# Performance work log

Measured on AMD Instinct MI355X. Metric: run time of the kernel, lower is better.

The kernel has to match this reference:

```python
import jax, jax.numpy as jnp
import numpy as np

B, C, H, W = 2, 256, 64, 64
D = 4  # max dilation ring


def _offsets():
    offs = [(0, 0)]
    for s in range(1, D + 1):
        for a in (-s, 0, s):
            for b in (-s, 0, s):
                if a != 0 or b != 0:
                    offs.append((a, b))
    return np.array(offs, dtype=np.int32)  # (33, 2)


def setup_inputs() -> dict:
    key = jax.random.key(0)
    k1, k2, k3, k4 = jax.random.split(key, 4)
    scale = 1.0 / np.sqrt(C)
    return {
        "Ft": jax.random.normal(k1, (B, C, H, W), dtype=jnp.float32),
        "Ft_epsilon": jax.random.normal(k2, (B, C, H, W), dtype=jnp.float32),
        "Wf": jax.random.normal(k3, (256, C), dtype=jnp.float32) * scale,
        "bf": jnp.zeros((256,), dtype=jnp.float32),
        "Wg": jax.random.normal(k4, (256, C), dtype=jnp.float32) * scale,
        "bg": jnp.zeros((256,), dtype=jnp.float32),
    }


def reference(Ft, Ft_epsilon, Wf, bf, Wg, bg):
    # 1x1 conv embeddings
    Ef = jnp.einsum("bchw,oc->bohw", Ft, Wf) + bf[None, :, None, None]          # f(Ft)
    Eg = jnp.einsum("bchw,oc->bohw", Ft_epsilon, Wg) + bg[None, :, None, None]  # g(Ft_eps)

    offs = _offsets()                                  # (K,2), K=33
    dx = jnp.asarray(offs[:, 0])[:, None, None]        # (K,1,1)
    dy = jnp.asarray(offs[:, 1])[:, None, None]
    xs = jnp.arange(H)[None, :, None] + dx             # (K,H,1)
    ys = jnp.arange(W)[None, None, :] + dy             # (K,1,W)
    valid = ((xs >= 0) & (xs < H)) & ((ys >= 0) & (ys < W))  # (K,H,W)
    xc = jnp.clip(xs, 0, H - 1)
    yc = jnp.clip(ys, 0, W - 1)

    # gather neighbor embeddings and features: (B,C,K,H,W)
    Ef_n = Ef[:, :, xc, yc]
    Ft_n = Ft[:, :, xc, yc]

    # affinity of center embedding with each neighbor embedding
    aff = jnp.einsum("bchw,bckhw->bkhw", Eg, Ef_n)     # (B,K,H,W)
    aff = jnp.where(valid[None], aff, -jnp.inf)        # clip out-of-bounds neighbors
    w = jax.nn.softmax(aff, axis=1)                    # (B,K,H,W); center always valid

    out = jnp.einsum("bkhw,bckhw->bchw", w, Ft_n)      # (B,C,H,W)
    return out
```

## Files before the change

kernel.cpp:

```cpp
#include <hip/hip_runtime.h>
#include <math.h>

typedef __attribute__((ext_vector_type(4))) float f4;

__device__ __forceinline__ int iclamp(int x, int lo, int hi) { return min(max(x, lo), hi); }

__device__ constexpr int DXC[33] = {0, -1,-1,-1,0,0,1,1,1, -2,-2,-2,0,0,2,2,2, -3,-3,-3,0,0,3,3,3, -4,-4,-4,0,0,4,4,4};
__device__ constexpr int DYC[33] = {0, -1,0,1,-1,1,-1,0,1, -2,0,2,-2,2,-2,0,2, -3,0,3,-3,3,-3,0,3, -4,0,4,-4,4,-4,0,4};

__global__ __launch_bounds__(256) void mat_M(
    const float* __restrict__ Wf, const float* __restrict__ Wg,
    const float* __restrict__ bg, float* __restrict__ Mt, float* __restrict__ r)
{
    __shared__ float Sf[32][33], Sg[32][33];
    __shared__ float Rs[32][9];
    const int c1b = blockIdx.x * 32, c2b = blockIdx.y * 32;
    const int tid = threadIdx.x;
    const int tx = tid & 15, ty = tid >> 4;
    float acc[2][2] = {};
    for (int ko = 0; ko < 256; ko += 32) {
        #pragma unroll
        for (int i = 0; i < 4; ++i) {
            int f = i * 256 + tid, o = f >> 5, c = f & 31;
            Sf[o][c] = Wf[(ko + o) * 256 + c1b + c];
            Sg[o][c] = Wg[(ko + o) * 256 + c2b + c];
        }
        __syncthreads();
        #pragma unroll
        for (int o = 0; o < 32; ++o) {
            float f0 = Sf[o][ty * 2], f1 = Sf[o][ty * 2 + 1];
            float g0 = Sg[o][tx * 2], g1 = Sg[o][tx * 2 + 1];
            acc[0][0] += f0 * g0; acc[0][1] += f0 * g1;
            acc[1][0] += f1 * g0; acc[1][1] += f1 * g1;
        }
        __syncthreads();
    }
    #pragma unroll
    for (int i = 0; i < 2; ++i)
        #pragma unroll
        for (int j = 0; j < 2; ++j)
            Mt[(size_t)(c2b + tx * 2 + j) * 256 + c1b + ty * 2 + i] = acc[i][j];

    if (blockIdx.y == 0) {
        const int c1l = tid & 31, og = tid >> 5;
        float s = 0.f;
        #pragma unroll 8
        for (int o = og * 32; o < og * 32 + 32; ++o)
            s += Wf[o * 256 + c1b + c1l] * bg[o];
        Rs[c1l][og] = s;
        __syncthreads();
        if (tid < 32) {
            float t = 0.f;
            #pragma unroll
            for (int j = 0; j < 8; ++j) t += Rs[tid][j];
            r[c1b + tid] = t;
        }
    }
}

__global__ __launch_bounds__(256, 2) void gemm_G(
    const float* __restrict__ Mt, const float* __restrict__ r,
    const float* __restrict__ FtE, float* __restrict__ G)
{
    __shared__ float Ms[256][64];
    const int bid = blockIdx.x;
    const int bn = bid & 63, bm = (bid >> 6) & 3, b = bid >> 8;
    const int tid = threadIdx.x;
    const int tn = tid & 15, tm = tid >> 4;
    const int m0 = bm * 64;
    const int m0g = m0 + tm * 4;
    const int n0g = bn * 64 + tn * 4;
    const float* X = FtE + (size_t)b * 1048576 + n0g;

    #pragma unroll
    for (int i = 0; i < 16; ++i) {
        int f = i * 256 + tid;
        int k = f >> 4, mi = f & 15;
        *(f4*)&Ms[k][mi * 4] = *(const f4*)&Mt[(size_t)k * 256 + m0 + mi * 4];
    }
    __syncthreads();

    f4 acc0 = {0.f,0.f,0.f,0.f}, acc1 = acc0, acc2 = acc0, acc3 = acc0;

    for (int kc = 0; kc < 256; kc += 8) {
        f4 x0 = *(const f4*)(X + (size_t)(kc + 0) * 4096);
        f4 x1 = *(const f4*)(X + (size_t)(kc + 1) * 4096);
        f4 x2 = *(const f4*)(X + (size_t)(kc + 2) * 4096);
        f4 x3 = *(const f4*)(X + (size_t)(kc + 3) * 4096);
        f4 x4 = *(const f4*)(X + (size_t)(kc + 4) * 4096);
        f4 x5 = *(const f4*)(X + (size_t)(kc + 5) * 4096);
        f4 x6 = *(const f4*)(X + (size_t)(kc + 6) * 4096);
        f4 x7 = *(const f4*)(X + (size_t)(kc + 7) * 4096);
        f4 a0 = *(const f4*)&Ms[kc + 0][tm * 4];
        f4 a1 = *(const f4*)&Ms[kc + 1][tm * 4];
        f4 a2 = *(const f4*)&Ms[kc + 2][tm * 4];
        f4 a3 = *(const f4*)&Ms[kc + 3][tm * 4];
        f4 a4 = *(const f4*)&Ms[kc + 4][tm * 4];
        f4 a5 = *(const f4*)&Ms[kc + 5][tm * 4];
        f4 a6 = *(const f4*)&Ms[kc + 6][tm * 4];
        f4 a7 = *(const f4*)&Ms[kc + 7][tm * 4];
        acc0 += x0 * a0.x; acc1 += x0 * a0.y; acc2 += x0 * a0.z; acc3 += x0 * a0.w;
        acc0 += x1 * a1.x; acc1 += x1 * a1.y; acc2 += x1 * a1.z; acc3 += x1 * a1.w;
        acc0 += x2 * a2.x; acc1 += x2 * a2.y; acc2 += x2 * a2.z; acc3 += x2 * a2.w;
        acc0 += x3 * a3.x; acc1 += x3 * a3.y; acc2 += x3 * a3.z; acc3 += x3 * a3.w;
        acc0 += x4 * a4.x; acc1 += x4 * a4.y; acc2 += x4 * a4.z; acc3 += x4 * a4.w;
        acc0 += x5 * a5.x; acc1 += x5 * a5.y; acc2 += x5 * a5.z; acc3 += x5 * a5.w;
        acc0 += x6 * a6.x; acc1 += x6 * a6.y; acc2 += x6 * a6.z; acc3 += x6 * a6.w;
        acc0 += x7 * a7.x; acc1 += x7 * a7.y; acc2 += x7 * a7.z; acc3 += x7 * a7.w;
    }

    float* Gp = G + (size_t)b * 1048576;
    {
        f4 v;
        v = acc0 + r[m0g + 0]; *(f4*)&Gp[(size_t)(m0g + 0) * 4096 + n0g] = v;
        v = acc1 + r[m0g + 1]; *(f4*)&Gp[(size_t)(m0g + 1) * 4096 + n0g] = v;
        v = acc2 + r[m0g + 2]; *(f4*)&Gp[(size_t)(m0g + 2) * 4096 + n0g] = v;
        v = acc3 + r[m0g + 3]; *(f4*)&Gp[(size_t)(m0g + 3) * 4096 + n0g] = v;
    }
}

template<bool LO, bool HI>
__device__ __forceinline__ void ldwin(float* wn, const float* Lb, int rd, int ch, int wq) {
    const float* p = &Lb[(rd * 8 + ch) * 72 + wq * 4];
    if constexpr (LO) { f4 v = *(const f4*)p;       wn[0]=v.x; wn[1]=v.y; wn[2]=v.z;  wn[3]=v.w; }
    {                   f4 v = *(const f4*)(p + 4); wn[4]=v.x; wn[5]=v.y; wn[6]=v.z;  wn[7]=v.w; }
    if constexpr (HI) { f4 v = *(const f4*)(p + 8); wn[8]=v.x; wn[9]=v.y; wn[10]=v.z; wn[11]=v.w; }
}

template<int DY>
__device__ __forceinline__ void fmadd4(f4& a, const f4& eg, const float* wn) {
    a.x += eg.x * wn[4 + DY];
    a.y += eg.y * wn[5 + DY];
    a.z += eg.z * wn[6 + DY];
    a.w += eg.w * wn[7 + DY];
}

template<int KQ>
__device__ __forceinline__ void aff_compute(const float* Lb, int wq, int cg, f4* acc)
{
    #pragma unroll
    for (int chi = 0; chi < 2; ++chi) {
        const int ch = cg * 2 + chi;
        f4 eg = *(const f4*)&Lb[(72 + ch) * 72 + 4 + wq * 4];
        float wn[12];
        if constexpr (KQ == 0) {
            ldwin<true,true>(wn, Lb, 0, ch, wq);
            fmadd4<-4>(acc[0], eg, wn); fmadd4<0>(acc[1], eg, wn); fmadd4<4>(acc[2], eg, wn);
            ldwin<true,true>(wn, Lb, 1, ch, wq);
            fmadd4<-3>(acc[3], eg, wn); fmadd4<0>(acc[4], eg, wn); fmadd4<3>(acc[5], eg, wn);
            ldwin<true,true>(wn, Lb, 2, ch, wq);
            fmadd4<-2>(acc[6], eg, wn); fmadd4<0>(acc[7], eg, wn); fmadd4<2>(acc[8], eg, wn);
        } else if constexpr (KQ == 1) {
            ldwin<true,true>(wn, Lb, 3, ch, wq);
            fmadd4<-1>(acc[0], eg, wn); fmadd4<0>(acc[1], eg, wn); fmadd4<1>(acc[2], eg, wn);
            ldwin<true,false>(wn, Lb, 4, ch, wq);
            fmadd4<-1>(acc[3], eg, wn); fmadd4<-2>(acc[4], eg, wn);
            fmadd4<-3>(acc[5], eg, wn); fmadd4<-4>(acc[6], eg, wn);
        } else if constexpr (KQ == 2) {
            ldwin<false,true>(wn, Lb, 4, ch, wq);
            fmadd4<0>(acc[0], eg, wn); fmadd4<1>(acc[1], eg, wn); fmadd4<2>(acc[2], eg, wn);
            fmadd4<3>(acc[3], eg, wn); fmadd4<4>(acc[4], eg, wn);
            ldwin<true,true>(wn, Lb, 5, ch, wq);
            fmadd4<-1>(acc[5], eg, wn); fmadd4<0>(acc[6], eg, wn); fmadd4<1>(acc[7], eg, wn);
        } else {
            ldwin<true,true>(wn, Lb, 6, ch, wq);
            fmadd4<-2>(acc[0], eg, wn); fmadd4<0>(acc[1], eg, wn); fmadd4<2>(acc[2], eg, wn);
            ldwin<true,true>(wn, Lb, 7, ch, wq);
            fmadd4<-3>(acc[3], eg, wn); fmadd4<0>(acc[4], eg, wn); fmadd4<3>(acc[5], eg, wn);
            ldwin<true,true>(wn, Lb, 8, ch, wq);
            fmadd4<-4>(acc[6], eg, wn); fmadd4<0>(acc[7], eg, wn); fmadd4<4>(acc[8], eg, wn);
        }
    }
}

__global__ __launch_bounds__(256, 2) void aff_part(
    const float* __restrict__ Ftg, const float* __restrict__ Gc,
    float* __restrict__ part)
{
    __shared__ float L[2][10 * 8 * 72];

    const int h = blockIdx.x, b = blockIdx.y, cseg = blockIdx.z;
    const int tid = threadIdx.x;
    const int wq = tid & 15, cg = (tid >> 4) & 3, kq = tid >> 6;
    const size_t plane = (size_t)b * 256 * 4096;
    const float* FtB = Ftg + plane;
    const float* GB  = Gc + plane;
    const int cbase = cseg * 64;

    int hr[10];
    #pragma unroll
    for (int d = 0; d < 10; ++d) hr[d] = (d < 9) ? iclamp(h + d - 4, 0, 63) : h;

    f4 vreg[5]; float sreg[3];

    auto load_rnd = [&](int rr) {
        const int c0 = cbase + rr * 8;
        #pragma unroll
        for (int i = 0; i < 5; ++i) {
            int f = i * 256 + tid, d = f >> 7, rem = f & 127, ch = rem >> 4, c4 = rem & 15;
            const float* src = (d < 9) ? FtB : GB;
            vreg[i] = *(const f4*)&src[(size_t)(c0 + ch) * 4096 + hr[d] * 64 + c4 * 4];
        }
        #pragma unroll
        for (int i = 0; i < 3; ++i) {
            int e = i * 256 + tid;
            if (e < 640) {
                int row = e >> 3, sc = e & 7, d = row >> 3, ch = row & 7;
                int wsrc = (sc < 4) ? 0 : 63;
                const float* src = (d < 9) ? FtB : GB;
                sreg[i] = src[(size_t)(c0 + ch) * 4096 + hr[d] * 64 + wsrc];
            }
        }
    };
    auto store_rnd = [&](int buf) {
        float* Lb = L[buf];
        #pragma unroll
        for (int i = 0; i < 5; ++i) {
            int f = i * 256 + tid, d = f >> 7, rem = f & 127, ch = rem >> 4, c4 = rem & 15;
            *(f4*)&Lb[(d * 8 + ch) * 72 + 4 + c4 * 4] = vreg[i];
        }
        #pragma unroll
        for (int i = 0; i < 3; ++i) {
            int e = i * 256 + tid;
            if (e < 640) {
                int row = e >> 3, sc = e & 7, d = row >> 3, ch = row & 7;
                int col = (sc < 4) ? sc : (64 + sc);
                Lb[(d * 8 + ch) * 72 + col] = sreg[i];
            }
        }
    };

    f4 acc[9] = {};

    load_rnd(0); store_rnd(0);
    for (int rr = 0; rr < 8; ++rr) {
        if (rr < 7) load_rnd(rr + 1);
        __syncthreads();
        const float* Lb = L[rr & 1];
        switch (kq) {
            case 0: aff_compute<0>(Lb, wq, cg, acc); break;
            case 1: aff_compute<1>(Lb, wq, cg, acc); break;
            case 2: aff_compute<2>(Lb, wq, cg, acc); break;
            default: aff_compute<3>(Lb, wq, cg, acc); break;
        }
        if (rr < 7) store_rnd((rr + 1) & 1);
    }

    #pragma unroll
    for (int j = 0; j < 9; ++j) {
        acc[j].x += __shfl_xor(acc[j].x, 16); acc[j].x += __shfl_xor(acc[j].x, 32);
        acc[j].y += __shfl_xor(acc[j].y, 16); acc[j].y += __shfl_xor(acc[j].y, 32);
        acc[j].z += __shfl_xor(acc[j].z, 16); acc[j].z += __shfl_xor(acc[j].z, 32);
        acc[j].w += __shfl_xor(acc[j].w, 16); acc[j].w += __shfl_xor(acc[j].w, 32);
    }

    if (cg == 0) {
        float* pB = part + (((size_t)cseg * 2 + b) * 33) * 4096 + h * 64 + wq * 4;
        #define STP(K, J) *(f4*)&pB[(size_t)(K) * 4096] = acc[J];
        switch (kq) {
            case 0: STP(25,0) STP(26,1) STP(27,2) STP(17,3) STP(18,4) STP(19,5) STP(9,6) STP(10,7) STP(11,8) break;
            case 1: STP(1,0) STP(2,1) STP(3,2) STP(4,3) STP(12,4) STP(20,5) STP(28,6) break;
            case 2: STP(0,0) STP(5,1) STP(13,2) STP(21,3) STP(29,4) STP(6,5) STP(7,6) STP(8,7) break;
            default: STP(14,0) STP(15,1) STP(16,2) STP(22,3) STP(23,4) STP(24,5) STP(30,6) STP(31,7) STP(32,8) break;
        }
        #undef STP
    }
}

__global__ __launch_bounds__(256, 2) void out_kernel(
    const float* __restrict__ part, const float* __restrict__ Ft,
    float* __restrict__ out)
{
    __shared__ float L[2][9 * 8 * 72];

    const int h = blockIdx.x, b = blockIdx.y, cseg = blockIdx.z;
    const int tid = threadIdx.x;
    const int w = tid & 63, cg = tid >> 6;
    const size_t plane = (size_t)b * 256 * 4096;
    const float* FtB = Ft + plane;
    float* outB = out + plane;
    const int cbase = cseg * 64;
    const int p = h * 64 + w;

    int hr[9];
    #pragma unroll
    for (int d = 0; d < 9; ++d) hr[d] = iclamp(h + d - 4, 0, 63);

    f4 vreg[5]; float sreg[3];

    auto load_rnd = [&](int rr) {
        const int c0 = cbase + rr * 8;
        #pragma unroll
        for (int i = 0; i < 5; ++i) {
            int f = i * 256 + tid;
            if (f < 1152) {
                int d = f >> 7, rem = f & 127, ch = rem >> 4, c4 = rem & 15;
                vreg[i] = *(const f4*)&FtB[(size_t)(c0 + ch) * 4096 + hr[d] * 64 + c4 * 4];
            }
        }
        #pragma unroll
        for (int i = 0; i < 3; ++i) {
            int e = i * 256 + tid;
            if (e < 576) {
                int row = e >> 3, sc = e & 7, d = row >> 3, ch = row & 7;
                int wsrc = (sc < 4) ? 0 : 63;
                sreg[i] = FtB[(size_t)(c0 + ch) * 4096 + hr[d] * 64 + wsrc];
            }
        }
    };
    auto store_rnd = [&](int buf) {
        float* Lb = L[buf];
        #pragma unroll
        for (int i = 0; i < 5; ++i) {
            int f = i * 256 + tid;
            if (f < 1152) {
                int d = f >> 7, rem = f & 127, ch = rem >> 4, c4 = rem & 15;
                *(f4*)&Lb[(d * 8 + ch) * 72 + 4 + c4 * 4] = vreg[i];
            }
        }
        #pragma unroll
        for (int i = 0; i < 3; ++i) {
            int e = i * 256 + tid;
            if (e < 576) {
                int row = e >> 3, sc = e & 7, d = row >> 3, ch = row & 7;
                int col = (sc < 4) ? sc : (64 + sc);
                Lb[(d * 8 + ch) * 72 + col] = sreg[i];
            }
        }
    };

    load_rnd(0);

    float wv[33];
    {
        constexpr size_t CS = (size_t)2 * 33 * 4096;
        const float* pB = part + ((size_t)b * 33) * 4096 + p;
        float mx = -INFINITY;
        #pragma unroll
        for (int k = 0; k < 33; ++k) {
            size_t off = (size_t)k * 4096;
            float s = pB[off] + pB[CS + off] + pB[2 * CS + off] + pB[3 * CS + off];
            bool valid = ((unsigned)(h + DXC[k]) < 64u) && ((unsigned)(w + DYC[k]) < 64u);
            wv[k] = valid ? s : -INFINITY;
            mx = fmaxf(mx, wv[k]);
        }
        float ssum = 0.f;
        #pragma unroll
        for (int k = 0; k < 33; ++k) { float e = __expf(wv[k] - mx); wv[k] = e; ssum += e; }
        float inv = 1.0f / ssum;
        #pragma unroll
        for (int k = 0; k < 33; ++k) wv[k] *= inv;
    }

    store_rnd(0);
    for (int rr = 0; rr < 8; ++rr) {
        if (rr < 7) load_rnd(rr + 1);
        __syncthreads();
        const float* base = &L[rr & 1][4 + w];
        #pragma unroll
        for (int u = 0; u < 2; ++u) {
            const float* b2 = base + (cg * 2 + u) * 72;
            float o = 0.f;
            #pragma unroll
            for (int k = 0; k < 33; ++k)
                o += wv[k] * b2[(DXC[k] + 4) * 576 + DYC[k]];
            int c = cbase + rr * 8 + cg * 2 + u;
            outB[(size_t)c * 4096 + p] = o;
        }
        if (rr < 7) store_rnd((rr + 1) & 1);
    }
}

extern "C" void kernel_launch(void* const* d_in, const int* in_sizes, int n_in,
                              void* d_out, int out_size, void* d_ws, size_t ws_size,
                              hipStream_t stream) {
    const float* Ft  = (const float*)d_in[0];
    const float* FtE = (const float*)d_in[1];
    const float* Wf  = (const float*)d_in[2];
    const float* bf  = (const float*)d_in[3];
    const float* Wg  = (const float*)d_in[4];
    const float* bg  = (const float*)d_in[5];
    float* out = (float*)d_out;
    (void)bf;

    float* G    = (float*)d_ws;
    float* part = G + (size_t)2 * 256 * 4096;
    float* Mt   = part + (size_t)4 * 2 * 33 * 4096;
    float* rw   = Mt + 256 * 256;

    hipLaunchKernelGGL(mat_M,      dim3(8, 8),     dim3(256), 0, stream, Wf, Wg, bg, Mt, rw);
    hipLaunchKernelGGL(gemm_G,     dim3(512),      dim3(256), 0, stream, Mt, rw, FtE, G);
    hipLaunchKernelGGL(aff_part,   dim3(64, 2, 4), dim3(256), 0, stream, Ft, G, part);
    hipLaunchKernelGGL(out_kernel, dim3(64, 2, 4), dim3(256), 0, stream, part, Ft, out);
}
```

Measured before the change: 144.5 us.

## Fuse G projection GEMM into affinity kernel, keeping G tile in shared memory

The separate gemm_G kernel is removed. Each affinity block now computes its own 64-channel by 64-pixel row tile of G in shared memory, and that tile feeds the affinity accumulation directly. This drops the global write and read of the full G tensor and one kernel launch. Shared-memory layout is reorganised into 16K floats, so occupancy and the tile shape are unchanged. In exchange, the GEMM now runs inside only 512 blocks, each of which loads the 64-column slice of Mt.

```diff
diff --git a/kernel.cpp b/kernel.cpp
--- a/kernel.cpp
+++ b/kernel.cpp
@@ -58,67 +58,6 @@
     }
 }
 
-__global__ __launch_bounds__(256, 2) void gemm_G(
-    const float* __restrict__ Mt, const float* __restrict__ r,
-    const float* __restrict__ FtE, float* __restrict__ G)
-{
-    __shared__ float Ms[256][64];
-    const int bid = blockIdx.x;
-    const int bn = bid & 63, bm = (bid >> 6) & 3, b = bid >> 8;
-    const int tid = threadIdx.x;
-    const int tn = tid & 15, tm = tid >> 4;
-    const int m0 = bm * 64;
-    const int m0g = m0 + tm * 4;
-    const int n0g = bn * 64 + tn * 4;
-    const float* X = FtE + (size_t)b * 1048576 + n0g;
-
-    #pragma unroll
-    for (int i = 0; i < 16; ++i) {
-        int f = i * 256 + tid;
-        int k = f >> 4, mi = f & 15;
-        *(f4*)&Ms[k][mi * 4] = *(const f4*)&Mt[(size_t)k * 256 + m0 + mi * 4];
-    }
-    __syncthreads();
-
-    f4 acc0 = {0.f,0.f,0.f,0.f}, acc1 = acc0, acc2 = acc0, acc3 = acc0;
-
-    for (int kc = 0; kc < 256; kc += 8) {
-        f4 x0 = *(const f4*)(X + (size_t)(kc + 0) * 4096);
-        f4 x1 = *(const f4*)(X + (size_t)(kc + 1) * 4096);
-        f4 x2 = *(const f4*)(X + (size_t)(kc + 2) * 4096);
-        f4 x3 = *(const f4*)(X + (size_t)(kc + 3) * 4096);
-        f4 x4 = *(const f4*)(X + (size_t)(kc + 4) * 4096);
-        f4 x5 = *(const f4*)(X + (size_t)(kc + 5) * 4096);
-        f4 x6 = *(const f4*)(X + (size_t)(kc + 6) * 4096);
-        f4 x7 = *(const f4*)(X + (size_t)(kc + 7) * 4096);
-        f4 a0 = *(const f4*)&Ms[kc + 0][tm * 4];
-        f4 a1 = *(const f4*)&Ms[kc + 1][tm * 4];
-        f4 a2 = *(const f4*)&Ms[kc + 2][tm * 4];
-        f4 a3 = *(const f4*)&Ms[kc + 3][tm * 4];
-        f4 a4 = *(const f4*)&Ms[kc + 4][tm * 4];
-        f4 a5 = *(const f4*)&Ms[kc + 5][tm * 4];
-        f4 a6 = *(const f4*)&Ms[kc + 6][tm * 4];
-        f4 a7 = *(const f4*)&Ms[kc + 7][tm * 4];
-        acc0 += x0 * a0.x; acc1 += x0 * a0.y; acc2 += x0 * a0.z; acc3 += x0 * a0.w;
-        acc0 += x1 * a1.x; acc1 += x1 * a1.y; acc2 += x1 * a1.z; acc3 += x1 * a1.w;
-        acc0 += x2 * a2.x; acc1 += x2 * a2.y; acc2 += x2 * a2.z; acc3 += x2 * a2.w;
-        acc0 += x3 * a3.x; acc1 += x3 * a3.y; acc2 += x3 * a3.z; acc3 += x3 * a3.w;
-        acc0 += x4 * a4.x; acc1 += x4 * a4.y; acc2 += x4 * a4.z; acc3 += x4 * a4.w;
-        acc0 += x5 * a5.x; acc1 += x5 * a5.y; acc2 += x5 * a5.z; acc3 += x5 * a5.w;
-        acc0 += x6 * a6.x; acc1 += x6 * a6.y; acc2 += x6 * a6.z; acc3 += x6 * a6.w;
-        acc0 += x7 * a7.x; acc1 += x7 * a7.y; acc2 += x7 * a7.z; acc3 += x7 * a7.w;
-    }
-
-    float* Gp = G + (size_t)b * 1048576;
-    {
-        f4 v;
-        v = acc0 + r[m0g + 0]; *(f4*)&Gp[(size_t)(m0g + 0) * 4096 + n0g] = v;
-        v = acc1 + r[m0g + 1]; *(f4*)&Gp[(size_t)(m0g + 1) * 4096 + n0g] = v;
-        v = acc2 + r[m0g + 2]; *(f4*)&Gp[(size_t)(m0g + 2) * 4096 + n0g] = v;
-        v = acc3 + r[m0g + 3]; *(f4*)&Gp[(size_t)(m0g + 3) * 4096 + n0g] = v;
-    }
-}
-
 template<bool LO, bool HI>
 __device__ __forceinline__ void ldwin(float* wn, const float* Lb, int rd, int ch, int wq) {
     const float* p = &Lb[(rd * 8 + ch) * 72 + wq * 4];
@@ -136,12 +75,13 @@
 }
 
 template<int KQ>
-__device__ __forceinline__ void aff_compute(const float* Lb, int wq, int cg, f4* acc)
+__device__ __forceinline__ void aff_compute(const float* Lb, const float* egb,
+                                            int wq, int cg, f4* acc)
 {
     #pragma unroll
     for (int chi = 0; chi < 2; ++chi) {
         const int ch = cg * 2 + chi;
-        f4 eg = *(const f4*)&Lb[(72 + ch) * 72 + 4 + wq * 4];
+        f4 eg = *(const f4*)&egb[ch * 68 + wq * 4];
         float wn[12];
         if constexpr (KQ == 0) {
             ldwin<true,true>(wn, Lb, 0, ch, wq);
@@ -173,23 +113,76 @@
     }
 }
 
-__global__ __launch_bounds__(256, 2) void aff_part(
-    const float* __restrict__ Ftg, const float* __restrict__ Gc,
+__global__ __launch_bounds__(256, 2) void gemm_aff(
+    const float* __restrict__ Mt, const float* __restrict__ rw,
+    const float* __restrict__ FtE, const float* __restrict__ Ftg,
     float* __restrict__ part)
 {
-    __shared__ float L[2][10 * 8 * 72];
-
+    __shared__ float SH[16384];
     const int h = blockIdx.x, b = blockIdx.y, cseg = blockIdx.z;
     const int tid = threadIdx.x;
+
+    float* Gs = SH;
+    float* L0 = SH + 4352;
+
+    {
+        float* Ms = SH;
+        const int tn = tid & 15, tm = tid >> 4;
+        const int m0 = cseg * 64;
+        const float* X = FtE + (size_t)b * 1048576 + h * 64 + tn * 4;
+
+        #pragma unroll
+        for (int i = 0; i < 16; ++i) {
+            int f = i * 256 + tid;
+            int k = f >> 4, mi = f & 15;
+            *(f4*)&Ms[k * 64 + mi * 4] = *(const f4*)&Mt[(size_t)k * 256 + m0 + mi * 4];
+        }
+        __syncthreads();
+
+        f4 acc0 = {0.f,0.f,0.f,0.f}, acc1 = acc0, acc2 = acc0, acc3 = acc0;
+        for (int kc = 0; kc < 256; kc += 8) {
+            f4 x0 = *(const f4*)(X + (size_t)(kc + 0) * 4096);
+            f4 x1 = *(const f4*)(X + (size_t)(kc + 1) * 4096);
+            f4 x2 = *(const f4*)(X + (size_t)(kc + 2) * 4096);
+            f4 x3 = *(const f4*)(X + (size_t)(kc + 3) * 4096);
+            f4 x4 = *(const f4*)(X + (size_t)(kc + 4) * 4096);
+            f4 x5 = *(const f4*)(X + (size_t)(kc + 5) * 4096);
+            f4 x6 = *(const f4*)(X + (size_t)(kc + 6) * 4096);
+            f4 x7 = *(const f4*)(X + (size_t)(kc + 7) * 4096);
+            f4 a0 = *(const f4*)&Ms[(kc + 0) * 64 + tm * 4];
+            f4 a1 = *(const f4*)&Ms[(kc + 1) * 64 + tm * 4];
+            f4 a2 = *(const f4*)&Ms[(kc + 2) * 64 + tm * 4];
+            f4 a3 = *(const f4*)&Ms[(kc + 3) * 64 + tm * 4];
+            f4 a4 = *(const f4*)&Ms[(kc + 4) * 64 + tm * 4];
+            f4 a5 = *(const f4*)&Ms[(kc + 5) * 64 + tm * 4];
+            f4 a6 = *(const f4*)&Ms[(kc + 6) * 64 + tm * 4];
+            f4 a7 = *(const f4*)&Ms[(kc + 7) * 64 + tm * 4];
+            acc0 += x0 * a0.x; acc1 += x0 * a0.y; acc2 += x0 * a0.z; acc3 += x0 * a0.w;
+            acc0 += x1 * a1.x; acc1 += x1 * a1.y; acc2 += x1 * a1.z; acc3 += x1 * a1.w;
+            acc0 += x2 * a2.x; acc1 += x2 * a2.y; acc2 += x2 * a2.z; acc3 += x2 * a2.w;
+            acc0 += x3 * a3.x; acc1 += x3 * a3.y; acc2 += x3 * a3.z; acc3 += x3 * a3.w;
+            acc0 += x4 * a4.x; acc1 += x4 * a4.y; acc2 += x4 * a4.z; acc3 += x4 * a4.w;
+            acc0 += x5 * a5.x; acc1 += x5 * a5.y; acc2 += x5 * a5.z; acc3 += x5 * a5.w;
+            acc0 += x6 * a6.x; acc1 += x6 * a6.y; acc2 += x6 * a6.z; acc3 += x6 * a6.w;
+            acc0 += x7 * a7.x; acc1 += x7 * a7.y; acc2 += x7 * a7.z; acc3 += x7 * a7.w;
+        }
+        __syncthreads();
+
+        const int m0g = m0 + tm * 4;
+        f4 v;
+        v = acc0 + rw[m0g + 0]; *(f4*)&Gs[(tm * 4 + 0) * 68 + tn * 4] = v;
+        v = acc1 + rw[m0g + 1]; *(f4*)&Gs[(tm * 4 + 1) * 68 + tn * 4] = v;
+        v = acc2 + rw[m0g + 2]; *(f4*)&Gs[(tm * 4 + 2) * 68 + tn * 4] = v;
+        v = acc3 + rw[m0g + 3]; *(f4*)&Gs[(tm * 4 + 3) * 68 + tn * 4] = v;
+    }
+
     const int wq = tid & 15, cg = (tid >> 4) & 3, kq = tid >> 6;
-    const size_t plane = (size_t)b * 256 * 4096;
-    const float* FtB = Ftg + plane;
-    const float* GB  = Gc + plane;
+    const float* FtB = Ftg + (size_t)b * 1048576;
     const int cbase = cseg * 64;
 
-    int hr[10];
-    #pragma unroll
-    for (int d = 0; d < 10; ++d) hr[d] = (d < 9) ? iclamp(h + d - 4, 0, 63) : h;
+    int hr[9];
+    #pragma unroll
+    for (int d = 0; d < 9; ++d) hr[d] = iclamp(h + d - 4, 0, 63);
 
     f4 vreg[5]; float sreg[3];
 
@@ -197,32 +190,36 @@
         const int c0 = cbase + rr * 8;
         #pragma unroll
         for (int i = 0; i < 5; ++i) {
-            int f = i * 256 + tid, d = f >> 7, rem = f & 127, ch = rem >> 4, c4 = rem & 15;
-            const float* src = (d < 9) ? FtB : GB;
-            vreg[i] = *(const f4*)&src[(size_t)(c0 + ch) * 4096 + hr[d] * 64 + c4 * 4];
+            int f = i * 256 + tid;
+            if (f < 1152) {
+                int d = f >> 7, rem = f & 127, ch = rem >> 4, c4 = rem & 15;
+                vreg[i] = *(const f4*)&FtB[(size_t)(c0 + ch) * 4096 + hr[d] * 64 + c4 * 4];
+            }
         }
         #pragma unroll
         for (int i = 0; i < 3; ++i) {
             int e = i * 256 + tid;
-            if (e < 640) {
+            if (e < 576) {
                 int row = e >> 3, sc = e & 7, d = row >> 3, ch = row & 7;
                 int wsrc = (sc < 4) ? 0 : 63;
-                const float* src = (d < 9) ? FtB : GB;
-                sreg[i] = src[(size_t)(c0 + ch) * 4096 + hr[d] * 64 + wsrc];
+                sreg[i] = FtB[(size_t)(c0 + ch) * 4096 + hr[d] * 64 + wsrc];
             }
         }
     };
     auto store_rnd = [&](int buf) {
-        float* Lb = L[buf];
+        float* Lb = L0 + buf * 5184;
         #pragma unroll
         for (int i = 0; i < 5; ++i) {
-            int f = i * 256 + tid, d = f >> 7, rem = f & 127, ch = rem >> 4, c4 = rem & 15;
-            *(f4*)&Lb[(d * 8 + ch) * 72 + 4 + c4 * 4] = vreg[i];
+            int f = i * 256 + tid;
+            if (f < 1152) {
+                int d = f >> 7, rem = f & 127, ch = rem >> 4, c4 = rem & 15;
+                *(f4*)&Lb[(d * 8 + ch) * 72 + 4 + c4 * 4] = vreg[i];
+            }
         }
         #pragma unroll
         for (int i = 0; i < 3; ++i) {
             int e = i * 256 + tid;
-            if (e < 640) {
+            if (e < 576) {
                 int row = e >> 3, sc = e & 7, d = row >> 3, ch = row & 7;
                 int col = (sc < 4) ? sc : (64 + sc);
                 Lb[(d * 8 + ch) * 72 + col] = sreg[i];
@@ -236,12 +233,13 @@
     for (int rr = 0; rr < 8; ++rr) {
         if (rr < 7) load_rnd(rr + 1);
         __syncthreads();
-        const float* Lb = L[rr & 1];
+        const float* Lb = L0 + (rr & 1) * 5184;
+        const float* egb = Gs + rr * 8 * 68;
         switch (kq) {
-            case 0: aff_compute<0>(Lb, wq, cg, acc); break;
-            case 1: aff_compute<1>(Lb, wq, cg, acc); break;
-            case 2: aff_compute<2>(Lb, wq, cg, acc); break;
-            default: aff_compute<3>(Lb, wq, cg, acc); break;
+            case 0: aff_compute<0>(Lb, egb, wq, cg, acc); break;
+            case 1: aff_compute<1>(Lb, egb, wq, cg, acc); break;
+            case 2: aff_compute<2>(Lb, egb, wq, cg, acc); break;
+            default: aff_compute<3>(Lb, egb, wq, cg, acc); break;
         }
         if (rr < 7) store_rnd((rr + 1) & 1);
     }
@@ -383,13 +381,11 @@
     float* out = (float*)d_out;
     (void)bf;
 
-    float* G    = (float*)d_ws;
-    float* part = G + (size_t)2 * 256 * 4096;
+    float* part = (float*)d_ws;
     float* Mt   = part + (size_t)4 * 2 * 33 * 4096;
     float* rw   = Mt + 256 * 256;
 
     hipLaunchKernelGGL(mat_M,      dim3(8, 8),     dim3(256), 0, stream, Wf, Wg, bg, Mt, rw);
-    hipLaunchKernelGGL(gemm_G,     dim3(512),      dim3(256), 0, stream, Mt, rw, FtE, G);
-    hipLaunchKernelGGL(aff_part,   dim3(64, 2, 4), dim3(256), 0, stream, Ft, G, part);
+    hipLaunchKernelGGL(gemm_aff,   dim3(64, 2, 4), dim3(256), 0, stream, Mt, rw, FtE, Ft, part);
     hipLaunchKernelGGL(out_kernel, dim3(64, 2, 4), dim3(256), 0, stream, part, Ft, out);
 }
```

Result: faster. 141.2 us (median of 2 runs) (-2.3%).
